# Kernel tuning notes

Hardware: AMD Instinct MI355X
Metric: run time of the kernel (lower is better)

The kernel has to match this reference:

```python
import jax, jax.numpy as jnp
import numpy as np

N_NODES = 50000
N_EDGES = 800000
IN_CH = 64
HID = 128


def setup_inputs() -> dict:
    key = jax.random.key(0)
    ks = jax.random.split(key, 8)
    s = 0.05
    x = jax.random.normal(ks[0], (N_NODES, IN_CH), dtype=jnp.float32)
    edge_index = jax.random.randint(ks[1], (2, N_EDGES), 0, N_NODES, dtype=jnp.int64)
    return {
        "x": x,
        "edge_index": edge_index,
        "W1l": jax.random.normal(ks[2], (HID, IN_CH), dtype=jnp.float32) * s,
        "b1l": jnp.zeros((HID,), dtype=jnp.float32),
        "W1r": jax.random.normal(ks[3], (HID, IN_CH), dtype=jnp.float32) * s,
        "W2l": jax.random.normal(ks[4], (HID, HID), dtype=jnp.float32) * s,
        "b2l": jnp.zeros((HID,), dtype=jnp.float32),
        "W2r": jax.random.normal(ks[5], (HID, HID), dtype=jnp.float32) * s,
        "Wrec": jax.random.normal(ks[6], (IN_CH, HID), dtype=jnp.float32) * s,
        "brec": jnp.zeros((IN_CH,), dtype=jnp.float32),
    }


def _sage_conv(x, src, dst, Wl, bl, Wr, n_nodes):
    # mean aggregation of source features at destination nodes
    msg_sum = jax.ops.segment_sum(x[src], dst, num_segments=n_nodes)  # [N, d]
    deg = jax.ops.segment_sum(jnp.ones((src.shape[0],), x.dtype), dst,
                              num_segments=n_nodes)  # [N]
    mean = msg_sum / jnp.maximum(deg, 1.0)[:, None]
    # SAGEConv: lin_l(aggr) + lin_r(x_i); lin_l has bias, lin_r does not
    return mean @ Wl.T + bl + x @ Wr.T


def reference(x, edge_index, W1l, b1l, W1r, W2l, b2l, W2r, Wrec, brec):
    src, dst = edge_index[0], edge_index[1]
    n = x.shape[0]
    h = _sage_conv(x, src, dst, W1l, b1l, W1r, n)
    h = jax.nn.relu(h)  # activation between layers, none after last
    z = _sage_conv(h, src, dst, W2l, b2l, W2r, n)
    x_recon = z @ Wrec.T + brec
    return (z, x_recon)
```

## Files before the change

kernel.cpp:

```cpp
#include <hip/hip_runtime.h>

#define N_NODES 50000
#define N_EDGES 800000
#define IN_CH 64
#define HID 128
#define NB_SCAN ((N_NODES + 255) / 256)


__global__ __launch_bounds__(256) void k_deg(const int* __restrict__ ei, int* __restrict__ deg) {
    int e = blockIdx.x * 256 + threadIdx.x;
    if (e < N_EDGES) {
        int d = ei[N_EDGES + e];
        if ((unsigned)d < N_NODES) atomicAdd(&deg[d], 1);
    }
}

__global__ __launch_bounds__(256) void k_scan1(const int* __restrict__ deg,
                                               int* __restrict__ excl,
                                               int* __restrict__ bsum) {
    int gid = blockIdx.x * 256 + threadIdx.x;
    int v = (gid < N_NODES) ? deg[gid] : 0;
    int lane = threadIdx.x & 63, wv = threadIdx.x >> 6;
    int s = v;
    #pragma unroll
    for (int d = 1; d < 64; d <<= 1) {
        int t = __shfl_up(s, d);
        if (lane >= d) s += t;
    }
    __shared__ int wsum[4];
    if (lane == 63) wsum[wv] = s;
    __syncthreads();
    int add = 0;
    #pragma unroll
    for (int w = 0; w < 4; w++) add += (w < wv) ? wsum[w] : 0;
    s += add;
    if (gid < N_NODES) excl[gid] = s - v;
    if (threadIdx.x == 255) bsum[blockIdx.x] = s;
}

__global__ __launch_bounds__(256) void k_scan2(const int* __restrict__ bsum,
                                               int* __restrict__ bpre,
                                               int* __restrict__ offs) {
    int tid = threadIdx.x;
    int v = (tid < NB_SCAN) ? bsum[tid] : 0;
    int lane = tid & 63, wv = tid >> 6;
    int s = v;
    #pragma unroll
    for (int d = 1; d < 64; d <<= 1) {
        int t = __shfl_up(s, d);
        if (lane >= d) s += t;
    }
    __shared__ int wsum[4];
    if (lane == 63) wsum[wv] = s;
    __syncthreads();
    int add = 0;
    #pragma unroll
    for (int w = 0; w < 4; w++) add += (w < wv) ? wsum[w] : 0;
    s += add;
    if (tid < NB_SCAN) bpre[tid] = s - v;
    if (tid == NB_SCAN - 1) offs[N_NODES] = s;
}

__global__ __launch_bounds__(256) void k_scan3(const int* __restrict__ excl,
                                               const int* __restrict__ bpre,
                                               int* __restrict__ offs) {
    int gid = blockIdx.x * 256 + threadIdx.x;
    if (gid < N_NODES) offs[gid] = excl[gid] + bpre[blockIdx.x];
}

__global__ __launch_bounds__(256) void k_fill(const int* __restrict__ ei, const int* __restrict__ offs,
                                              int* __restrict__ cursor, int* __restrict__ csr) {
    int e = blockIdx.x * 256 + threadIdx.x;
    if (e < N_EDGES) {
        int s = ei[e];
        int d = ei[N_EDGES + e];
        if ((unsigned)d < N_NODES && (unsigned)s < N_NODES) {
            int pos = atomicAdd(&cursor[d], 1);
            csr[offs[d] + pos] = s;
        }
    }
}


template <int CH>
__global__ __launch_bounds__(256) void k_agg(const float* __restrict__ feat,
                                             const int* __restrict__ csr,
                                             const int* __restrict__ offs,
                                             float* __restrict__ meanout) {
    int wid = (blockIdx.x * 256 + threadIdx.x) >> 6;
    int lane = threadIdx.x & 63;
    if (wid >= N_NODES) return;
    int beg = offs[wid], end = offs[wid + 1];
    int degn = end - beg;
    float inv = 1.0f / (float)(degn > 0 ? degn : 1);

    if (CH == 64) {
        float s = 0.f;
        int e = beg;
        for (; e + 4 <= end; e += 4) {
            int i0 = csr[e], i1 = csr[e + 1], i2 = csr[e + 2], i3 = csr[e + 3];
            float a = feat[i0 * 64 + lane];
            float b = feat[i1 * 64 + lane];
            float c = feat[i2 * 64 + lane];
            float d = feat[i3 * 64 + lane];
            s += a + b + c + d;
        }
        for (; e < end; e++) s += feat[csr[e] * 64 + lane];
        meanout[wid * 64 + lane] = s * inv;
    } else {
        const float2* F = (const float2*)feat;
        float sx = 0.f, sy = 0.f;
        int e = beg;
        for (; e + 4 <= end; e += 4) {
            int i0 = csr[e], i1 = csr[e + 1], i2 = csr[e + 2], i3 = csr[e + 3];
            float2 a = F[i0 * 64 + lane];
            float2 b = F[i1 * 64 + lane];
            float2 c = F[i2 * 64 + lane];
            float2 d = F[i3 * 64 + lane];
            sx += a.x + b.x + c.x + d.x;
            sy += a.y + b.y + c.y + d.y;
        }
        for (; e < end; e++) { float2 a = F[csr[e] * 64 + lane]; sx += a.x; sy += a.y; }
        float2 r; r.x = sx * inv; r.y = sy * inv;
        ((float2*)meanout)[wid * 64 + lane] = r;
    }
}


template <int NOUT, int KTOT, bool DUAL, bool RELU>
__global__ __launch_bounds__(256) void k_gemm(const float* __restrict__ A0, const float* __restrict__ A1,
                                              const float* __restrict__ W0, const float* __restrict__ W1,
                                              const float* __restrict__ bias, float* __restrict__ out) {
    constexpr int K1 = DUAL ? KTOT / 2 : KTOT;
    constexpr int KC = 32;
    constexpr int NCH = KTOT / KC;
    constexpr int NJ = NOUT / 8;
    constexpr int MP = 64 * NJ / 256;
    constexpr int ASTR = 36;
    constexpr int WSTR = (NOUT == 128) ? 140 : 68;

    __shared__ float As[64 * ASTR];
    __shared__ float Ws[KC * WSTR];

    int tid = threadIdx.x;
    int tx = tid % NJ;
    int ty = tid / NJ;
    int m0 = blockIdx.x * 64;

    float acc[MP][8];
    #pragma unroll
    for (int i = 0; i < MP; i++)
        #pragma unroll
        for (int j = 0; j < 8; j++) acc[i][j] = 0.f;

    for (int ch = 0; ch < NCH; ch++) {
        int k0 = ch * KC;
        const float* Ap; const float* Wp; int ak0;
        if (DUAL && k0 >= K1) { Ap = A1; Wp = W1; ak0 = k0 - K1; }
        else                  { Ap = A0; Wp = W0; ak0 = k0; }

        __syncthreads();
        #pragma unroll
        for (int it = 0; it < 2; it++) {
            int idx = tid + it * 256;
            int n = idx >> 3, sl = idx & 7;
            int gn = m0 + n;
            float4 v = make_float4(0.f, 0.f, 0.f, 0.f);
            if (gn < N_NODES) v = *(const float4*)(Ap + (size_t)gn * K1 + ak0 + sl * 4);
            *(float4*)(As + n * ASTR + sl * 4) = v;
        }
        #pragma unroll
        for (int it = 0; it < NOUT * KC / 4 / 256; it++) {
            int idx = tid + it * 256;
            int sl = idx & 7, jj = idx >> 3;
            float4 w = *(const float4*)(Wp + jj * K1 + ak0 + sl * 4);
            int cb = jj + ((jj >> 5) << 2);
            Ws[(sl * 4 + 0) * WSTR + cb] = w.x;
            Ws[(sl * 4 + 1) * WSTR + cb] = w.y;
            Ws[(sl * 4 + 2) * WSTR + cb] = w.z;
            Ws[(sl * 4 + 3) * WSTR + cb] = w.w;
        }
        __syncthreads();

        #pragma unroll
        for (int k = 0; k < KC; k++) {
            float a[MP];
            #pragma unroll
            for (int mi = 0; mi < MP; mi++) {
                int n = ty * MP + mi;
                a[mi] = As[n * ASTR + k];
            }
            const float* wr = Ws + k * WSTR + tx * 8 + ((tx >> 2) << 2);
            float4 w0 = *(const float4*)wr;
            float4 w1 = *(const float4*)(wr + 4);
            #pragma unroll
            for (int mi = 0; mi < MP; mi++) {
                acc[mi][0] += a[mi] * w0.x;
                acc[mi][1] += a[mi] * w0.y;
                acc[mi][2] += a[mi] * w0.z;
                acc[mi][3] += a[mi] * w0.w;
                acc[mi][4] += a[mi] * w1.x;
                acc[mi][5] += a[mi] * w1.y;
                acc[mi][6] += a[mi] * w1.z;
                acc[mi][7] += a[mi] * w1.w;
            }
        }
    }

    int jb = tx * 8;
    float4 bv0 = *(const float4*)(bias + jb);
    float4 bv1 = *(const float4*)(bias + jb + 4);
    #pragma unroll
    for (int mi = 0; mi < MP; mi++) {
        int gn = m0 + ty * MP + mi;
        if (gn < N_NODES) {
            float4 r0, r1;
            r0.x = acc[mi][0] + bv0.x; r0.y = acc[mi][1] + bv0.y;
            r0.z = acc[mi][2] + bv0.z; r0.w = acc[mi][3] + bv0.w;
            r1.x = acc[mi][4] + bv1.x; r1.y = acc[mi][5] + bv1.y;
            r1.z = acc[mi][6] + bv1.z; r1.w = acc[mi][7] + bv1.w;
            if (RELU) {
                r0.x = fmaxf(r0.x, 0.f); r0.y = fmaxf(r0.y, 0.f);
                r0.z = fmaxf(r0.z, 0.f); r0.w = fmaxf(r0.w, 0.f);
                r1.x = fmaxf(r1.x, 0.f); r1.y = fmaxf(r1.y, 0.f);
                r1.z = fmaxf(r1.z, 0.f); r1.w = fmaxf(r1.w, 0.f);
            }
            *(float4*)(out + (size_t)gn * NOUT + jb) = r0;
            *(float4*)(out + (size_t)gn * NOUT + jb + 4) = r1;
        }
    }
}


extern "C" void kernel_launch(void* const* d_in, const int* in_sizes, int n_in,
                              void* d_out, int out_size, void* d_ws, size_t ws_size,
                              hipStream_t stream) {
    const float* x    = (const float*)d_in[0];
    const int*   ei   = (const int*)d_in[1];
    const float* W1l  = (const float*)d_in[2];
    const float* b1l  = (const float*)d_in[3];
    const float* W1r  = (const float*)d_in[4];
    const float* W2l  = (const float*)d_in[5];
    const float* b2l  = (const float*)d_in[6];
    const float* W2r  = (const float*)d_in[7];
    const float* Wrec = (const float*)d_in[8];
    const float* brec = (const float*)d_in[9];

    float* z    = (float*)d_out;
    float* xrec = (float*)d_out + (size_t)N_NODES * HID;

    char* ws = (char*)d_ws;
    int*   deg    = (int*)(ws);
    int*   offs   = (int*)(ws + (256u << 10));
    int*   cursor = (int*)(ws + (512u << 10));
    int*   excl   = (int*)(ws + (768u << 10));
    int*   bsum   = (int*)(ws + (1024u << 10));
    int*   bpre   = (int*)(ws + (1028u << 10));
    int*   csr    = (int*)(ws + (2u << 20));
    float* mean1  = (float*)(ws + (6u << 20));
    float* mean2  = (float*)(ws + (6u << 20));
    float* h      = (float*)(ws + (32u << 20));

    hipMemsetAsync(deg, 0, N_NODES * sizeof(int), stream);
    hipMemsetAsync(cursor, 0, N_NODES * sizeof(int), stream);

    int egrid = (N_EDGES + 255) / 256;
    int ngrid = (N_NODES + 63) / 64;

    k_deg<<<egrid, 256, 0, stream>>>(ei, deg);
    k_scan1<<<NB_SCAN, 256, 0, stream>>>(deg, excl, bsum);
    k_scan2<<<1, 256, 0, stream>>>(bsum, bpre, offs);
    k_scan3<<<NB_SCAN, 256, 0, stream>>>(excl, bpre, offs);
    k_fill<<<egrid, 256, 0, stream>>>(ei, offs, cursor, csr);

    k_agg<64><<<N_NODES / 4, 256, 0, stream>>>(x, csr, offs, mean1);
    k_gemm<128, 128, true, true><<<ngrid, 256, 0, stream>>>(mean1, x, W1l, W1r, b1l, h);
    k_agg<128><<<N_NODES / 4, 256, 0, stream>>>(h, csr, offs, mean2);
    k_gemm<128, 256, true, false><<<ngrid, 256, 0, stream>>>(mean2, h, W2l, W2r, b2l, z);
    k_gemm<64, 128, false, false><<<ngrid, 256, 0, stream>>>(z, nullptr, Wrec, nullptr, brec, xrec);
}
```

Baseline: 365.8 us.

## Switch features and weights to bf16 and use MFMA GEMMs

Converts the input features and all weight matrices to bf16 up front. Gather-mean aggregation then reads and writes bf16 rows, which halves gather bandwidth. The shared-memory FP32 GEMMs are replaced by MFMA bf16 16x16x32 kernels that load operands straight from global memory. The hidden activations h and z are stored as bf16 intermediates, and z is still written in fp32 for output. This reduces precision of intermediates and outputs, and adds conversion kernels.

```diff
diff --git a/kernel.cpp b/kernel.cpp
--- a/kernel.cpp
+++ b/kernel.cpp
@@ -5,6 +5,47 @@
 #define IN_CH 64
 #define HID 128
 #define NB_SCAN ((N_NODES + 255) / 256)
+
+typedef short short8 __attribute__((ext_vector_type(8)));
+typedef float f32x4 __attribute__((ext_vector_type(4)));
+
+static __device__ __forceinline__ unsigned short f2bf(float f) {
+    unsigned u = __float_as_uint(f);
+    u += 0x7FFF + ((u >> 16) & 1);
+    return (unsigned short)(u >> 16);
+}
+static __device__ __forceinline__ float bflo(unsigned v) { return __uint_as_float(v << 16); }
+static __device__ __forceinline__ float bfhi(unsigned v) { return __uint_as_float(v & 0xFFFF0000u); }
+
+
+__global__ __launch_bounds__(256) void k_cvt(const float* __restrict__ src,
+                                             unsigned short* __restrict__ dst, int n4) {
+    int i = blockIdx.x * 256 + threadIdx.x;
+    if (i < n4) {
+        float4 v = ((const float4*)src)[i];
+        unsigned lo = f2bf(v.x) | ((unsigned)f2bf(v.y) << 16);
+        unsigned hi = f2bf(v.z) | ((unsigned)f2bf(v.w) << 16);
+        ((uint2*)dst)[i] = make_uint2(lo, hi);
+    }
+}
+
+__global__ __launch_bounds__(256) void k_cvt_w(const float* __restrict__ W1l, const float* __restrict__ W1r,
+                                               const float* __restrict__ W2l, const float* __restrict__ W2r,
+                                               const float* __restrict__ Wrec, unsigned short* __restrict__ dst) {
+    int i = blockIdx.x * 256 + threadIdx.x;
+    int e = i * 4;
+    if (e >= 57344) return;
+    const float* src; int off;
+    if (e < 8192)       { src = W1l;  off = 0; }
+    else if (e < 16384) { src = W1r;  off = 8192; }
+    else if (e < 32768) { src = W2l;  off = 16384; }
+    else if (e < 49152) { src = W2r;  off = 32768; }
+    else                { src = Wrec; off = 49152; }
+    float4 v = *(const float4*)(src + (e - off));
+    unsigned lo = f2bf(v.x) | ((unsigned)f2bf(v.y) << 16);
+    unsigned hi = f2bf(v.z) | ((unsigned)f2bf(v.w) << 16);
+    *(uint2*)(dst + e) = make_uint2(lo, hi);
+}
 
 
 __global__ __launch_bounds__(256) void k_deg(const int* __restrict__ ei, int* __restrict__ deg) {
@@ -81,152 +122,106 @@
     }
 }
 
-
-template <int CH>
-__global__ __launch_bounds__(256) void k_agg(const float* __restrict__ feat,
-                                             const int* __restrict__ csr,
-                                             const int* __restrict__ offs,
-                                             float* __restrict__ meanout) {
+__global__ __launch_bounds__(256) void k_agg64b(const unsigned short* __restrict__ X,
+                                                const int* __restrict__ csr,
+                                                const int* __restrict__ offs,
+                                                unsigned short* __restrict__ out) {
     int wid = (blockIdx.x * 256 + threadIdx.x) >> 6;
     int lane = threadIdx.x & 63;
     if (wid >= N_NODES) return;
     int beg = offs[wid], end = offs[wid + 1];
     int degn = end - beg;
     float inv = 1.0f / (float)(degn > 0 ? degn : 1);
-
-    if (CH == 64) {
-        float s = 0.f;
-        int e = beg;
-        for (; e + 4 <= end; e += 4) {
-            int i0 = csr[e], i1 = csr[e + 1], i2 = csr[e + 2], i3 = csr[e + 3];
-            float a = feat[i0 * 64 + lane];
-            float b = feat[i1 * 64 + lane];
-            float c = feat[i2 * 64 + lane];
-            float d = feat[i3 * 64 + lane];
-            s += a + b + c + d;
+    int half = lane >> 5, hl = lane & 31;
+    float sx = 0.f, sy = 0.f;
+    for (int e = beg + half; e < end; e += 2) {
+        int idx = csr[e];
+        unsigned v = *(const unsigned*)(X + (size_t)idx * 64 + hl * 2);
+        sx += bflo(v); sy += bfhi(v);
+    }
+    sx += __shfl_xor(sx, 32);
+    sy += __shfl_xor(sy, 32);
+    if (half == 0) {
+        unsigned o = f2bf(sx * inv) | ((unsigned)f2bf(sy * inv) << 16);
+        *(unsigned*)(out + (size_t)wid * 64 + hl * 2) = o;
+    }
+}
+
+__global__ __launch_bounds__(256) void k_agg128b(const unsigned short* __restrict__ X,
+                                                 const int* __restrict__ csr,
+                                                 const int* __restrict__ offs,
+                                                 unsigned short* __restrict__ out) {
+    int wid = (blockIdx.x * 256 + threadIdx.x) >> 6;
+    int lane = threadIdx.x & 63;
+    if (wid >= N_NODES) return;
+    int beg = offs[wid], end = offs[wid + 1];
+    int degn = end - beg;
+    float inv = 1.0f / (float)(degn > 0 ? degn : 1);
+    float sx = 0.f, sy = 0.f;
+    int e = beg;
+    for (; e + 2 <= end; e += 2) {
+        int i0 = csr[e], i1 = csr[e + 1];
+        unsigned a = *(const unsigned*)(X + (size_t)i0 * 128 + lane * 2);
+        unsigned b = *(const unsigned*)(X + (size_t)i1 * 128 + lane * 2);
+        sx += bflo(a) + bflo(b);
+        sy += bfhi(a) + bfhi(b);
+    }
+    if (e < end) {
+        unsigned a = *(const unsigned*)(X + (size_t)csr[e] * 128 + lane * 2);
+        sx += bflo(a); sy += bfhi(a);
+    }
+    unsigned o = f2bf(sx * inv) | ((unsigned)f2bf(sy * inv) << 16);
+    *(unsigned*)(out + (size_t)wid * 128 + lane * 2) = o;
+}
+
+
+template <int NOUT, int KTOT, bool DUAL, bool RELU, bool WF32, bool WBF16>
+__global__ __launch_bounds__(256) void k_gemm_mfma(const unsigned short* __restrict__ A0,
+                                                   const unsigned short* __restrict__ A1,
+                                                   const unsigned short* __restrict__ W0,
+                                                   const unsigned short* __restrict__ W1,
+                                                   const float* __restrict__ bias,
+                                                   float* __restrict__ out,
+                                                   unsigned short* __restrict__ outb) {
+    constexpr int K1 = DUAL ? KTOT / 2 : KTOT;
+    constexpr int NF = NOUT / 16;
+    int lane = threadIdx.x & 63;
+    int wv = threadIdx.x >> 6;
+    int m0 = blockIdx.x * 64 + wv * 16;
+    int arow = m0 + (lane & 15);
+    if (arow >= N_NODES) arow = N_NODES - 1;
+    int kg = lane >> 4;
+
+    f32x4 acc[NF] = {};
+
+    #pragma unroll
+    for (int ks = 0; ks < KTOT / 32; ks++) {
+        int k0 = ks * 32;
+        const unsigned short* Ap; const unsigned short* Wp; int kk;
+        if (DUAL && k0 >= K1) { Ap = A1; Wp = W1; kk = k0 - K1; }
+        else                  { Ap = A0; Wp = W0; kk = k0; }
+        short8 a = *(const short8*)(Ap + (size_t)arow * K1 + kk + kg * 8);
+        #pragma unroll
+        for (int j = 0; j < NF; j++) {
+            short8 b = *(const short8*)(Wp + (size_t)(j * 16 + (lane & 15)) * K1 + kk + kg * 8);
+            acc[j] = __builtin_amdgcn_mfma_f32_16x16x32_bf16(a, b, acc[j], 0, 0, 0);
         }
-        for (; e < end; e++) s += feat[csr[e] * 64 + lane];
-        meanout[wid * 64 + lane] = s * inv;
-    } else {
-        const float2* F = (const float2*)feat;
-        float sx = 0.f, sy = 0.f;
-        int e = beg;
-        for (; e + 4 <= end; e += 4) {
-            int i0 = csr[e], i1 = csr[e + 1], i2 = csr[e + 2], i3 = csr[e + 3];
-            float2 a = F[i0 * 64 + lane];
-            float2 b = F[i1 * 64 + lane];
-            float2 c = F[i2 * 64 + lane];
-            float2 d = F[i3 * 64 + lane];
-            sx += a.x + b.x + c.x + d.x;
-            sy += a.y + b.y + c.y + d.y;
-        }
-        for (; e < end; e++) { float2 a = F[csr[e] * 64 + lane]; sx += a.x; sy += a.y; }
-        float2 r; r.x = sx * inv; r.y = sy * inv;
-        ((float2*)meanout)[wid * 64 + lane] = r;
-    }
-}
-
-
-template <int NOUT, int KTOT, bool DUAL, bool RELU>
-__global__ __launch_bounds__(256) void k_gemm(const float* __restrict__ A0, const float* __restrict__ A1,
-                                              const float* __restrict__ W0, const float* __restrict__ W1,
-                                              const float* __restrict__ bias, float* __restrict__ out) {
-    constexpr int K1 = DUAL ? KTOT / 2 : KTOT;
-    constexpr int KC = 32;
-    constexpr int NCH = KTOT / KC;
-    constexpr int NJ = NOUT / 8;
-    constexpr int MP = 64 * NJ / 256;
-    constexpr int ASTR = 36;
-    constexpr int WSTR = (NOUT == 128) ? 140 : 68;
-
-    __shared__ float As[64 * ASTR];
-    __shared__ float Ws[KC * WSTR];
-
-    int tid = threadIdx.x;
-    int tx = tid % NJ;
-    int ty = tid / NJ;
-    int m0 = blockIdx.x * 64;
-
-    float acc[MP][8];
-    #pragma unroll
-    for (int i = 0; i < MP; i++)
+    }
+
+    int col = lane & 15;
+    int r0 = (lane >> 4) * 4;
+    #pragma unroll
+    for (int j = 0; j < NF; j++) {
+        float bv = bias[j * 16 + col];
         #pragma unroll
-        for (int j = 0; j < 8; j++) acc[i][j] = 0.f;
-
-    for (int ch = 0; ch < NCH; ch++) {
-        int k0 = ch * KC;
-        const float* Ap; const float* Wp; int ak0;
-        if (DUAL && k0 >= K1) { Ap = A1; Wp = W1; ak0 = k0 - K1; }
-        else                  { Ap = A0; Wp = W0; ak0 = k0; }
-
-        __syncthreads();
-        #pragma unroll
-        for (int it = 0; it < 2; it++) {
-            int idx = tid + it * 256;
-            int n = idx >> 3, sl = idx & 7;
-            int gn = m0 + n;
-            float4 v = make_float4(0.f, 0.f, 0.f, 0.f);
-            if (gn < N_NODES) v = *(const float4*)(Ap + (size_t)gn * K1 + ak0 + sl * 4);
-            *(float4*)(As + n * ASTR + sl * 4) = v;
-        }
-        #pragma unroll
-        for (int it = 0; it < NOUT * KC / 4 / 256; it++) {
-            int idx = tid + it * 256;
-            int sl = idx & 7, jj = idx >> 3;
-            float4 w = *(const float4*)(Wp + jj * K1 + ak0 + sl * 4);
-            int cb = jj + ((jj >> 5) << 2);
-            Ws[(sl * 4 + 0) * WSTR + cb] = w.x;
-            Ws[(sl * 4 + 1) * WSTR + cb] = w.y;
-            Ws[(sl * 4 + 2) * WSTR + cb] = w.z;
-            Ws[(sl * 4 + 3) * WSTR + cb] = w.w;
-        }
-        __syncthreads();
-
-        #pragma unroll
-        for (int k = 0; k < KC; k++) {
-            float a[MP];
-            #pragma unroll
-            for (int mi = 0; mi < MP; mi++) {
-                int n = ty * MP + mi;
-                a[mi] = As[n * ASTR + k];
+        for (int r = 0; r < 4; r++) {
+            int grow = m0 + r0 + r;
+            if (grow < N_NODES) {
+                float v = acc[j][r] + bv;
+                if (RELU) v = fmaxf(v, 0.f);
+                if (WF32)  out[(size_t)grow * NOUT + j * 16 + col] = v;
+                if (WBF16) outb[(size_t)grow * NOUT + j * 16 + col] = f2bf(v);
             }
-            const float* wr = Ws + k * WSTR + tx * 8 + ((tx >> 2) << 2);
-            float4 w0 = *(const float4*)wr;
-            float4 w1 = *(const float4*)(wr + 4);
-            #pragma unroll
-            for (int mi = 0; mi < MP; mi++) {
-                acc[mi][0] += a[mi] * w0.x;
-                acc[mi][1] += a[mi] * w0.y;
-                acc[mi][2] += a[mi] * w0.z;
-                acc[mi][3] += a[mi] * w0.w;
-                acc[mi][4] += a[mi] * w1.x;
-                acc[mi][5] += a[mi] * w1.y;
-                acc[mi][6] += a[mi] * w1.z;
-                acc[mi][7] += a[mi] * w1.w;
-            }
-        }
-    }
-
-    int jb = tx * 8;
-    float4 bv0 = *(const float4*)(bias + jb);
-    float4 bv1 = *(const float4*)(bias + jb + 4);
-    #pragma unroll
-    for (int mi = 0; mi < MP; mi++) {
-        int gn = m0 + ty * MP + mi;
-        if (gn < N_NODES) {
-            float4 r0, r1;
-            r0.x = acc[mi][0] + bv0.x; r0.y = acc[mi][1] + bv0.y;
-            r0.z = acc[mi][2] + bv0.z; r0.w = acc[mi][3] + bv0.w;
-            r1.x = acc[mi][4] + bv1.x; r1.y = acc[mi][5] + bv1.y;
-            r1.z = acc[mi][6] + bv1.z; r1.w = acc[mi][7] + bv1.w;
-            if (RELU) {
-                r0.x = fmaxf(r0.x, 0.f); r0.y = fmaxf(r0.y, 0.f);
-                r0.z = fmaxf(r0.z, 0.f); r0.w = fmaxf(r0.w, 0.f);
-                r1.x = fmaxf(r1.x, 0.f); r1.y = fmaxf(r1.y, 0.f);
-                r1.z = fmaxf(r1.z, 0.f); r1.w = fmaxf(r1.w, 0.f);
-            }
-            *(float4*)(out + (size_t)gn * NOUT + jb) = r0;
-            *(float4*)(out + (size_t)gn * NOUT + jb + 4) = r1;
         }
     }
 }
@@ -257,15 +252,27 @@
     int*   bsum   = (int*)(ws + (1024u << 10));
     int*   bpre   = (int*)(ws + (1028u << 10));
     int*   csr    = (int*)(ws + (2u << 20));
-    float* mean1  = (float*)(ws + (6u << 20));
-    float* mean2  = (float*)(ws + (6u << 20));
-    float* h      = (float*)(ws + (32u << 20));
+    unsigned short* wb     = (unsigned short*)(ws + (5632u << 10));
+    unsigned short* xb     = (unsigned short*)(ws + (7u  << 20));
+    unsigned short* hb     = (unsigned short*)(ws + (14u << 20));
+    unsigned short* mean1b = (unsigned short*)(ws + (27u << 20));
+    unsigned short* mean2b = (unsigned short*)(ws + (27u << 20));
+    unsigned short* zb     = (unsigned short*)(ws + (40u << 20));
+
+    unsigned short* W1lb  = wb;
+    unsigned short* W1rb  = wb + 8192;
+    unsigned short* W2lb  = wb + 16384;
+    unsigned short* W2rb  = wb + 32768;
+    unsigned short* Wrecb = wb + 49152;
 
     hipMemsetAsync(deg, 0, N_NODES * sizeof(int), stream);
     hipMemsetAsync(cursor, 0, N_NODES * sizeof(int), stream);
 
     int egrid = (N_EDGES + 255) / 256;
     int ngrid = (N_NODES + 63) / 64;
+
+    k_cvt_w<<<56, 256, 0, stream>>>(W1l, W1r, W2l, W2r, Wrec, wb);
+    k_cvt<<<(800000 + 255) / 256, 256, 0, stream>>>(x, xb, 800000);
 
     k_deg<<<egrid, 256, 0, stream>>>(ei, deg);
     k_scan1<<<NB_SCAN, 256, 0, stream>>>(deg, excl, bsum);
@@ -273,9 +280,12 @@
     k_scan3<<<NB_SCAN, 256, 0, stream>>>(excl, bpre, offs);
     k_fill<<<egrid, 256, 0, stream>>>(ei, offs, cursor, csr);
 
-    k_agg<64><<<N_NODES / 4, 256, 0, stream>>>(x, csr, offs, mean1);
-    k_gemm<128, 128, true, true><<<ngrid, 256, 0, stream>>>(mean1, x, W1l, W1r, b1l, h);
-    k_agg<128><<<N_NODES / 4, 256, 0, stream>>>(h, csr, offs, mean2);
-    k_gemm<128, 256, true, false><<<ngrid, 256, 0, stream>>>(mean2, h, W2l, W2r, b2l, z);
-    k_gemm<64, 128, false, false><<<ngrid, 256, 0, stream>>>(z, nullptr, Wrec, nullptr, brec, xrec);
-}
+    k_agg64b<<<N_NODES / 4, 256, 0, stream>>>(xb, csr, offs, mean1b);
+    k_gemm_mfma<128, 128, true, true, false, true>
+        <<<ngrid, 256, 0, stream>>>(mean1b, xb, W1lb, W1rb, b1l, nullptr, hb);
+    k_agg128b<<<N_NODES / 4, 256, 0, stream>>>(hb, csr, offs, mean2b);
+    k_gemm_mfma<128, 256, true, false, true, true>
+        <<<ngrid, 256, 0, stream>>>(mean2b, hb, W2lb, W2rb, b2l, z, zb);
+    k_gemm_mfma<64, 128, false, false, true, false>
+        <<<ngrid, 256, 0, stream>>>(zb, nullptr, Wrecb, nullptr, brec, xrec, nullptr);
+}
```

New measurement: 349.6 us. -4.4%, faster.
